# Kernel optimization log

Hardware: AMD Instinct MI355X
Metric: run time of the kernel (lower is better)

Reference implementation:

```python
import jax, jax.numpy as jnp
import numpy as np

M, K, D = 8, 4096, 512  # groups, codes per group, total dim
DG = D // M             # per-group dim = 64


def setup_inputs() -> dict:
    key = jax.random.key(0)
    k1, k2, k3 = jax.random.split(key, 3)
    codes = jax.random.randint(k1, (32, 64, 64, M), 0, K, dtype=jnp.int32)
    codebook = jax.random.normal(k2, (M, K, DG), dtype=jnp.float32)
    wv = jax.random.normal(k3, (M, DG, DG), dtype=jnp.float32) / np.sqrt(DG)
    return {"codes": codes, "codebook": codebook, "wv": wv}


def reference(codes, codebook, wv):
    # v[m,k,c] = sum_d codebook[m,k,d] * wv[m,c,d]  (small per-group GEMM)
    v = jnp.einsum('mkd,mcd->mkc', codebook, wv)  # [M, K, DG]
    # one-hot matmul over k is exactly an indexed gather:
    # gathered[n,h,w,m,c] = v[m, codes[n,h,w,m], c]
    m_idx = jnp.arange(v.shape[0])  # [M]
    gathered = v[m_idx[None, None, None, :], codes]  # [n,h,w,M,DG]
    n, h, w = codes.shape[:3]
    out = gathered.reshape(n, h, w, -1)          # [n,h,w,D]
    return jnp.transpose(out, (0, 3, 1, 2))      # [n,D,h,w]
```

## Files before the change

kernel.cpp:

```cpp
#include <hip/hip_runtime.h>
#include <hip/hip_bf16.h>

#define MQ 8
#define KQ 4096
#define DG 64
#define NN 32
#define HW 4096
#define DD 512

__global__ __launch_bounds__(256) void compute_v_kernel(
    const float* __restrict__ codebook,
    const float* __restrict__ wv,
    float* __restrict__ v) {
  __shared__ float wv_t[DG][DG + 1];
  __shared__ float cb[64][DG];

  const int m = blockIdx.y;
  const int k0 = blockIdx.x * 64;
  const int tid = threadIdx.x;

  const float* wvm = wv + (size_t)m * DG * DG;
  for (int i = tid; i < DG * DG; i += 256) {
    int c = i >> 6, d = i & 63;
    wv_t[d][c] = wvm[i];
  }
  const float* cbm = codebook + ((size_t)m * KQ + k0) * DG;
  for (int i = tid; i < 64 * DG; i += 256) {
    cb[i >> 6][i & 63] = cbm[i];
  }
  __syncthreads();

  const int c = tid & 63;
  const int kq = tid >> 6;

  float acc[16];
#pragma unroll
  for (int kl = 0; kl < 16; ++kl) acc[kl] = 0.f;

  for (int d = 0; d < DG; ++d) {
    float w = wv_t[d][c];
#pragma unroll
    for (int kl = 0; kl < 16; ++kl) {
      acc[kl] += cb[kq * 16 + kl][d] * w;
    }
  }

  float* vout = v + ((size_t)m * KQ + k0) * DG;
#pragma unroll
  for (int kl = 0; kl < 16; ++kl) {
    vout[(size_t)(kq * 16 + kl) * DG + c] = acc[kl];
  }
}

__global__ __launch_bounds__(256) void gather_kernel(
    const int* __restrict__ codes,
    const float* __restrict__ v,
    float* __restrict__ out) {
  const int b = blockIdx.x;
  const int m = b & 7;
  const int t = b >> 3;
  const int n = t & 31;
  const int chunk = t >> 5;
  const int hw = chunk * 1024 + threadIdx.x * 4;

  const int cbase = (n * HW + hw) * MQ + m;
  const int r0 = codes[cbase];
  const int r1 = codes[cbase + MQ];
  const int r2 = codes[cbase + 2 * MQ];
  const int r3 = codes[cbase + 3 * MQ];

  const float* vm = v + (size_t)m * KQ * DG;
  const float4* p0 = (const float4*)(vm + (size_t)r0 * DG);
  const float4* p1 = (const float4*)(vm + (size_t)r1 * DG);
  const float4* p2 = (const float4*)(vm + (size_t)r2 * DG);
  const float4* p3 = (const float4*)(vm + (size_t)r3 * DG);

  float* outbase = out + ((size_t)n * DD + m * DG) * HW + hw;

#pragma unroll 4
  for (int cg = 0; cg < 16; ++cg) {
    float4 a0 = p0[cg];
    float4 a1 = p1[cg];
    float4 a2 = p2[cg];
    float4 a3 = p3[cg];
    float4 w;
    w.x = a0.x; w.y = a1.x; w.z = a2.x; w.w = a3.x;
    *(float4*)(outbase + (size_t)(cg * 4 + 0) * HW) = w;
    w.x = a0.y; w.y = a1.y; w.z = a2.y; w.w = a3.y;
    *(float4*)(outbase + (size_t)(cg * 4 + 1) * HW) = w;
    w.x = a0.z; w.y = a1.z; w.z = a2.z; w.w = a3.z;
    *(float4*)(outbase + (size_t)(cg * 4 + 2) * HW) = w;
    w.x = a0.w; w.y = a1.w; w.z = a2.w; w.w = a3.w;
    *(float4*)(outbase + (size_t)(cg * 4 + 3) * HW) = w;
  }
}

extern "C" void kernel_launch(void* const* d_in, const int* in_sizes, int n_in,
                              void* d_out, int out_size, void* d_ws, size_t ws_size,
                              hipStream_t stream) {
  const int* codes = (const int*)d_in[0];
  const float* codebook = (const float*)d_in[1];
  const float* wv = (const float*)d_in[2];
  float* out = (float*)d_out;
  float* v = (float*)d_ws;

  compute_v_kernel<<<dim3(64, 8), 256, 0, stream>>>(codebook, wv, v);
  gather_kernel<<<1024, 256, 0, stream>>>(codes, v, out);
}
```

Before: 363.0 us.

## Stage gathered rows in shared memory and transpose with coalesced nontemporal stores

The gather kernel now loads each block's codes into shared memory, gathers 128 rows of v into a padded LDS tile with coalesced per-row reads, then writes the transposed output with coalesced scalar nontemporal stores. The grid grows from 1024 blocks to 8192. compute_v also switches to float4 global and LDS loads. The goal is better-coalesced gather reads and more parallelism, at the cost of two barriers and extra LDS traffic per block, and scalar stores in place of float4 stores.

```diff
diff --git a/kernel.cpp b/kernel.cpp
--- a/kernel.cpp
+++ b/kernel.cpp
@@ -7,6 +7,7 @@
 #define NN 32
 #define HW 4096
 #define DD 512
+#define THW 128
 
 __global__ __launch_bounds__(256) void compute_v_kernel(
     const float* __restrict__ codebook,
@@ -19,15 +20,18 @@
   const int k0 = blockIdx.x * 64;
   const int tid = threadIdx.x;
 
-  const float* wvm = wv + (size_t)m * DG * DG;
-  for (int i = tid; i < DG * DG; i += 256) {
-    int c = i >> 6, d = i & 63;
-    wv_t[d][c] = wvm[i];
+  const float4* wvm4 = (const float4*)(wv + (size_t)m * DG * DG);
+  for (int i = tid; i < DG * DG / 4; i += 256) {
+    int c = i >> 4, d4 = (i & 15) * 4;
+    float4 val = wvm4[i];
+    wv_t[d4 + 0][c] = val.x;
+    wv_t[d4 + 1][c] = val.y;
+    wv_t[d4 + 2][c] = val.z;
+    wv_t[d4 + 3][c] = val.w;
   }
-  const float* cbm = codebook + ((size_t)m * KQ + k0) * DG;
-  for (int i = tid; i < 64 * DG; i += 256) {
-    cb[i >> 6][i & 63] = cbm[i];
-  }
+  const float4* cbm4 = (const float4*)(codebook + ((size_t)m * KQ + k0) * DG);
+  float4* cb4 = (float4*)&cb[0][0];
+  for (int i = tid; i < 64 * DG / 4; i += 256) cb4[i] = cbm4[i];
   __syncthreads();
 
   const int c = tid & 63;
@@ -37,11 +41,15 @@
 #pragma unroll
   for (int kl = 0; kl < 16; ++kl) acc[kl] = 0.f;
 
-  for (int d = 0; d < DG; ++d) {
-    float w = wv_t[d][c];
+  for (int d4 = 0; d4 < DG; d4 += 4) {
+    float w0 = wv_t[d4 + 0][c];
+    float w1 = wv_t[d4 + 1][c];
+    float w2 = wv_t[d4 + 2][c];
+    float w3 = wv_t[d4 + 3][c];
 #pragma unroll
     for (int kl = 0; kl < 16; ++kl) {
-      acc[kl] += cb[kq * 16 + kl][d] * w;
+      float4 cbv = *(const float4*)&cb[kq * 16 + kl][d4];
+      acc[kl] += cbv.x * w0 + cbv.y * w1 + cbv.z * w2 + cbv.w * w3;
     }
   }
 
@@ -56,42 +64,45 @@
     const int* __restrict__ codes,
     const float* __restrict__ v,
     float* __restrict__ out) {
+  __shared__ int scode[THW];
+  __shared__ float tile[THW][DG + 1];
+
   const int b = blockIdx.x;
   const int m = b & 7;
   const int t = b >> 3;
   const int n = t & 31;
-  const int chunk = t >> 5;
-  const int hw = chunk * 1024 + threadIdx.x * 4;
+  const int tileidx = t >> 5;
+  const int hw0 = tileidx * THW;
 
-  const int cbase = (n * HW + hw) * MQ + m;
-  const int r0 = codes[cbase];
-  const int r1 = codes[cbase + MQ];
-  const int r2 = codes[cbase + 2 * MQ];
-  const int r3 = codes[cbase + 3 * MQ];
+  const int tid = threadIdx.x;
+  const int w = tid >> 6;
+  const int l = tid & 63;
+
+  if (tid < THW) {
+    scode[tid] = codes[((size_t)n * HW + hw0 + tid) * MQ + m];
+  }
+  __syncthreads();
 
   const float* vm = v + (size_t)m * KQ * DG;
-  const float4* p0 = (const float4*)(vm + (size_t)r0 * DG);
-  const float4* p1 = (const float4*)(vm + (size_t)r1 * DG);
-  const float4* p2 = (const float4*)(vm + (size_t)r2 * DG);
-  const float4* p3 = (const float4*)(vm + (size_t)r3 * DG);
+#pragma unroll 8
+  for (int jj = 0; jj < 32; ++jj) {
+    int j = w * 32 + jj;
+    int r = scode[j];
+    tile[j][l] = vm[(size_t)r * DG + l];
+  }
+  __syncthreads();
 
-  float* outbase = out + ((size_t)n * DD + m * DG) * HW + hw;
-
+  float* outb = out + ((size_t)n * DD + (size_t)m * DG) * HW + hw0;
 #pragma unroll 4
-  for (int cg = 0; cg < 16; ++cg) {
-    float4 a0 = p0[cg];
-    float4 a1 = p1[cg];
-    float4 a2 = p2[cg];
-    float4 a3 = p3[cg];
-    float4 w;
-    w.x = a0.x; w.y = a1.x; w.z = a2.x; w.w = a3.x;
-    *(float4*)(outbase + (size_t)(cg * 4 + 0) * HW) = w;
-    w.x = a0.y; w.y = a1.y; w.z = a2.y; w.w = a3.y;
-    *(float4*)(outbase + (size_t)(cg * 4 + 1) * HW) = w;
-    w.x = a0.z; w.y = a1.z; w.z = a2.z; w.w = a3.z;
-    *(float4*)(outbase + (size_t)(cg * 4 + 2) * HW) = w;
-    w.x = a0.w; w.y = a1.w; w.z = a2.w; w.w = a3.w;
-    *(float4*)(outbase + (size_t)(cg * 4 + 3) * HW) = w;
+  for (int u = 0; u < 16; ++u) {
+    int up = w * 16 + u;
+    int c = up >> 1;
+    int half = up & 1;
+    int j = half * 64 + l;
+    float val0 = tile[j][c];
+    float val1 = tile[j][c + 32];
+    __builtin_nontemporal_store(val0, outb + (size_t)c * HW + j);
+    __builtin_nontemporal_store(val1, outb + (size_t)(c + 32) * HW + j);
   }
 }
 
@@ -105,5 +116,5 @@
   float* v = (float*)d_ws;
 
   compute_v_kernel<<<dim3(64, 8), 256, 0, stream>>>(codebook, wv, v);
-  gather_kernel<<<1024, 256, 0, stream>>>(codes, v, out);
+  gather_kernel<<<NN * MQ * (HW / THW), 256, 0, stream>>>(codes, v, out);
 }
```

Measured after the change: 316.8 us. 1.15x faster.
